# Optimization experiments

Measured on AMD Instinct MI355X. Metric: run time of the kernel, lower is better.

## Reference

```python
import jax, jax.numpy as jnp
import numpy as np

N_NODES = 100000
N_REL = 8
IN_DIM = 64
HID = 128
OUT = 64
N_EDGES = 640000


def setup_inputs() -> dict:
    key = jax.random.key(0)
    ks = jax.random.split(key, 24)

    def w(k, shape, fan_in):
        return jax.random.normal(k, shape, jnp.float32) / np.sqrt(fan_in).astype(np.float32)

    inp = {}
    inp["emb"] = jax.random.normal(ks[0], (N_NODES, IN_DIM), jnp.float32)
    dims = [(IN_DIM, HID), (HID, HID), (HID, HID // 2), (HID // 2, OUT)]
    for i, (di, do) in enumerate(dims, 1):
        inp[f"W{i}"] = w(ks[3 * i], (N_REL, di, do), di)      # per-relation weight
        inp[f"R{i}"] = w(ks[3 * i + 1], (di, do), di)          # root weight
        inp[f"B{i}"] = jnp.zeros((do,), jnp.float32)           # bias
    inp["g1"] = jnp.ones((HID,), jnp.float32)
    inp["b1"] = jnp.zeros((HID,), jnp.float32)
    inp["g2"] = jnp.ones((HID,), jnp.float32)
    inp["b2"] = jnp.zeros((HID,), jnp.float32)
    inp["ei"] = jax.random.randint(ks[20], (2, N_EDGES), 0, N_NODES, jnp.int32)
    inp["et"] = jax.random.randint(ks[21], (N_EDGES,), 0, N_REL, jnp.int32)
    return inp


def rgcn(x, ei, et, W, Wr, b):
    # PyG RGCNConv (aggr='mean'): out_i = x_i @ Wroot + b + sum_r mean_{j in N_r(i)} x_j @ W_r
    # Aggregate-then-transform: mean x[src] per (dst, rel) bin, then per-relation GEMM.
    n, r, d = x.shape[0], W.shape[0], x.shape[1]
    src, dst = ei[0], ei[1]
    seg = dst * r + et                                   # combined (node, relation) segment id
    agg = jax.ops.segment_sum(x[src], seg, num_segments=n * r)          # [N*R, d]
    cnt = jax.ops.segment_sum(jnp.ones((src.shape[0],), x.dtype), seg, num_segments=n * r)
    agg = (agg / jnp.maximum(cnt, 1.0)[:, None]).reshape(n, r, d)       # mean per relation
    return jnp.einsum('nri,rio->no', agg, W) + x @ Wr + b


def layer_norm(x, g, b, eps=1e-5):
    mu = jnp.mean(x, axis=-1, keepdims=True)
    var = jnp.mean((x - mu) ** 2, axis=-1, keepdims=True)
    return (x - mu) * jax.lax.rsqrt(var + eps) * g + b


def reference(emb, W1, R1, B1, W2, R2, B2, W3, R3, B3, W4, R4, B4, g1, b1, g2, b2, ei, et):
    # dropout is eval-mode identity
    x = jax.nn.relu(rgcn(emb, ei, et, W1, R1, B1))
    x = layer_norm(x, g1, b1)
    identity = x
    x = jax.nn.relu(rgcn(x, ei, et, W2, R2, B2))
    x = layer_norm(x + identity, g2, b2)
    x = jax.nn.relu(rgcn(x, ei, et, W3, R3, B3))
    return rgcn(x, ei, et, W4, R4, B4)
```

## Files before the change

kernel.cpp:

```cpp
#include <hip/hip_runtime.h>
#include <math.h>

#define NN 100000
#define NR 8
#define NE 640000
#define SEGN (NN * NR)
#define SPB 2048
#define NSB ((SEGN + SPB - 1) / SPB)

#define TILES 1563
#define HT1 782
#define HT2 781
#define HP1 (HT1 * 64)
#define HP2 (HT2 * 64)
#define HPF (TILES * 64)

typedef __attribute__((ext_vector_type(8))) __bf16 bf16x8;
typedef __attribute__((ext_vector_type(4))) float  f32x4;

__device__ __forceinline__ float bf2f(unsigned short b) {
    return __uint_as_float((unsigned)b << 16);
}
__device__ __forceinline__ unsigned short f2bf(float v) {
    __bf16 b = (__bf16)v;
    return __builtin_bit_cast(unsigned short, b);
}


__global__ __launch_bounds__(256) void count_kernel(
    const int* __restrict__ dst, const int* __restrict__ et, unsigned* __restrict__ cnt) {
    int e = blockIdx.x * 256 + threadIdx.x;
    if (e < NE) atomicAdd(&cnt[(size_t)et[e] * NN + dst[e]], 1u);
}

__global__ __launch_bounds__(256) void scan1_kernel(
    const unsigned* __restrict__ cnt, unsigned* __restrict__ bsum) {
    __shared__ unsigned red[256];
    int b = blockIdx.x, t = threadIdx.x;
    int i0 = b * SPB;
    unsigned s = 0;
#pragma unroll
    for (int k = 0; k < SPB / 256; ++k) {
        int i = i0 + k * 256 + t;
        if (i < SEGN) s += cnt[i];
    }
    red[t] = s;
    __syncthreads();
    for (int off = 128; off >= 1; off >>= 1) {
        if (t < off) red[t] += red[t + off];
        __syncthreads();
    }
    if (t == 0) bsum[b] = red[0];
}

__global__ __launch_bounds__(512) void scan2_kernel(
    unsigned* __restrict__ bsum, int* __restrict__ segoff) {
    __shared__ unsigned buf[512];
    int t = threadIdx.x;
    unsigned v = (t < NSB) ? bsum[t] : 0u;
    buf[t] = v;
    __syncthreads();
    for (int off = 1; off < 512; off <<= 1) {
        unsigned w = (t >= off) ? buf[t - off] : 0u;
        __syncthreads();
        buf[t] += w;
        __syncthreads();
    }
    if (t < NSB) bsum[t] = buf[t] - v;
    if (t == 0) segoff[SEGN] = NE;
}

__global__ __launch_bounds__(256) void scan3_kernel(
    const unsigned* __restrict__ cnt, const unsigned* __restrict__ bsum,
    int* __restrict__ segoff) {
    __shared__ unsigned lc[SPB];
    __shared__ unsigned tsum[256];
    int b = blockIdx.x, t = threadIdx.x;
    int i0 = b * SPB;
#pragma unroll
    for (int k = 0; k < SPB / 256; ++k) {
        int i = i0 + k * 256 + t;
        lc[k * 256 + t] = (i < SEGN) ? cnt[i] : 0u;
    }
    __syncthreads();
    unsigned s = 0;
#pragma unroll
    for (int k = 0; k < 8; ++k) s += lc[t * 8 + k];
    tsum[t] = s;
    __syncthreads();
    for (int off = 1; off < 256; off <<= 1) {
        unsigned w = (t >= off) ? tsum[t - off] : 0u;
        __syncthreads();
        tsum[t] += w;
        __syncthreads();
    }
    unsigned base = bsum[b] + tsum[t] - s;
#pragma unroll
    for (int k = 0; k < 8; ++k) {
        unsigned c = lc[t * 8 + k];
        lc[t * 8 + k] = base;
        base += c;
    }
    __syncthreads();
#pragma unroll
    for (int k = 0; k < SPB / 256; ++k) {
        int i = i0 + k * 256 + t;
        if (i < SEGN) segoff[i] = (int)lc[k * 256 + t];
    }
}

__global__ __launch_bounds__(256) void fill_kernel(
    const int* __restrict__ src, const int* __restrict__ dst, const int* __restrict__ et,
    const int* __restrict__ segoff, unsigned* __restrict__ cursor, int* __restrict__ esrc) {
    int e = blockIdx.x * 256 + threadIdx.x;
    if (e >= NE) return;
    int d = dst[e];
    int seg = et[e] * NN + d;
    int pos = segoff[seg] + (int)atomicAdd(&cursor[seg], 1u);
    esrc[pos] = src[e] | ((d & 3) << 17);
}


template <int D, int O>
__global__ __launch_bounds__(256) void pack_kernel(
    const float* __restrict__ W, const float* __restrict__ Wr, __bf16* __restrict__ Wp) {
    constexpr int KT = D / 32, NTN = O / 16;
    int idx = blockIdx.x * 256 + threadIdx.x;
    if (idx >= (NR + 1) * KT * NTN * 64) return;
    int l = idx & 63;
    int rest = idx >> 6;
    int nt = rest % NTN; rest /= NTN;
    int kt = rest % KT;
    int r  = rest / KT;
    const float* srcw = (r < NR) ? (W + (size_t)r * D * O) : Wr;
    int n  = nt * 16 + (l & 15);
    int k0 = kt * 32 + (l >> 4) * 8;
    bf16x8 v;
#pragma unroll
    for (int j = 0; j < 8; ++j) {
        int p  = k0 + j;
        int kd = (D == 128) ? ((p >> 1) + ((p & 1) << 6)) : p;
        v[j] = (__bf16)srcw[(size_t)kd * O + n];
    }
    *(bf16x8*)(Wp + (size_t)idx * 8) = v;
}


template <int D, int XF>
__global__ __launch_bounds__(256) void gather_kernel(
    const void* __restrict__ xin, const int* __restrict__ segoff,
    const int* __restrict__ esrc, ushort* __restrict__ agg,
    int nbase, int agg_off, int HP)
{
    int wv = threadIdx.x >> 6, ln = threadIdx.x & 63;
    int r  = blockIdx.y;
    int i0 = blockIdx.x * 16 + wv * 4;
    int n0 = nbase + i0;

    const float*    xf = (const float*)xin;
    const ushort*   xb = (const ushort*)xin;
    const unsigned* xs = (const unsigned*)xin;

    float ax[4] = {0, 0, 0, 0}, ay[4] = {0, 0, 0, 0};
    int eo[5];
#pragma unroll
    for (int k = 0; k <= 4; ++k) {
        int node = n0 + k; if (node > NN) node = NN;
        eo[k] = segoff[r * NN + node];
    }
    for (int ei = eo[0]; ei < eo[4]; ei += 4) {
        int nb = eo[4] - ei; if (nb > 4) nb = 4;
        int mm[4]; float vx[4], vy[4];
#pragma unroll
        for (int b = 0; b < 4; ++b) mm[b] = (b < nb) ? esrc[ei + b] : 0;
#pragma unroll
        for (int b = 0; b < 4; ++b) {
            if (b < nb) {
                int s = mm[b] & 0x1FFFF;
                if constexpr (XF == 0) {
                    vx[b] = xf[(size_t)s * 64 + ln];
                } else if constexpr (XF == 1) {
                    unsigned w = xs[(size_t)s * 64 + ln];
                    vx[b] = bf2f((unsigned short)(w & 0xFFFFu));
                    vy[b] = bf2f((unsigned short)(w >> 16));
                } else {
                    vx[b] = bf2f(xb[(size_t)s * 64 + ln]);
                }
            }
        }
#pragma unroll
        for (int b = 0; b < 4; ++b) {
            if (b < nb) {
                int k = mm[b] >> 17;
#pragma unroll
                for (int kk = 0; kk < 4; ++kk) {
                    ax[kk] += (kk == k) ? vx[b] : 0.0f;
                    if constexpr (D == 128) ay[kk] += (kk == k) ? vy[b] : 0.0f;
                }
            }
        }
    }
#pragma unroll
    for (int k = 0; k < 4; ++k) {
        int c = eo[k + 1] - eo[k];
        float sc = (c > 0) ? 1.0f / (float)c : 0.0f;
        size_t row = ((size_t)r * HP + agg_off + i0 + k) * D;
        if constexpr (D == 128) {
            unsigned st = (unsigned)f2bf(ax[k] * sc) | ((unsigned)f2bf(ay[k] * sc) << 16);
            *((unsigned*)(agg + row) + ln) = st;
        } else {
            agg[row + ln] = f2bf(ax[k] * sc);
        }
    }
}


template <int D, int O, int MODE, int XF, int OF>
__global__ __launch_bounds__(256) void gemm_layer(
    const ushort* __restrict__ agg, const __bf16* __restrict__ Wp,
    const float* __restrict__ bias, const float* __restrict__ gamma,
    const float* __restrict__ beta, const unsigned* __restrict__ xres,
    const void* __restrict__ xroot, void* __restrict__ outv, int base, int HP)
{
    constexpr int KT = D / 32, NTN = O / 16;
    int t = threadIdx.x, wv = t >> 6, ln = t & 63, lg = ln >> 4, lm = ln & 15;
    int i0 = blockIdx.x * 64;

    f32x4 acc[NTN];
#pragma unroll
    for (int nt = 0; nt < NTN; ++nt)
#pragma unroll
        for (int q = 0; q < 4; ++q) acc[nt][q] = 0.0f;

    const ushort* abase = agg + ((size_t)(i0 + wv * 16 + lm)) * D + lg * 8;

#pragma unroll 1
    for (int r = 0; r < 8; ++r) {
        const ushort* ar = abase + (size_t)r * HP * D;
        const __bf16* bp = Wp + (((size_t)(r * KT) * NTN) << 9) + (ln << 3);
#pragma unroll
        for (int kt = 0; kt < KT; ++kt) {
            bf16x8 A = *(const bf16x8*)(ar + kt * 32);
            const __bf16* bpk = bp + (((size_t)(kt * NTN)) << 9);
#pragma unroll
            for (int nt = 0; nt < NTN; ++nt) {
                bf16x8 B = *(const bf16x8*)(bpk + ((size_t)nt << 9));
                acc[nt] = __builtin_amdgcn_mfma_f32_16x16x32_bf16(A, B, acc[nt], 0, 0, 0);
            }
        }
    }
    {
        int nrow = base + i0 + wv * 16 + lm;
        if (nrow >= NN) nrow = NN - 1;
        const __bf16* bp = Wp + (((size_t)(8 * KT) * NTN) << 9) + (ln << 3);
#pragma unroll
        for (int kt = 0; kt < KT; ++kt) {
            bf16x8 A;
            if constexpr (XF == 0) {
                const float* xp = (const float*)xroot + (size_t)nrow * 64 + kt * 32 + lg * 8;
                f32x4 a0 = *(const f32x4*)xp;
                f32x4 a1 = *(const f32x4*)(xp + 4);
#pragma unroll
                for (int j = 0; j < 4; ++j) { A[j] = (__bf16)a0[j]; A[j + 4] = (__bf16)a1[j]; }
            } else if constexpr (XF == 1) {
                A = *(const bf16x8*)((const ushort*)xroot + (size_t)nrow * 128 + kt * 32 + lg * 8);
            } else {
                A = *(const bf16x8*)((const ushort*)xroot + (size_t)nrow * 64 + kt * 32 + lg * 8);
            }
            const __bf16* bpk = bp + (((size_t)(kt * NTN)) << 9);
#pragma unroll
            for (int nt = 0; nt < NTN; ++nt) {
                bf16x8 B = *(const bf16x8*)(bpk + ((size_t)nt << 9));
                acc[nt] = __builtin_amdgcn_mfma_f32_16x16x32_bf16(A, B, acc[nt], 0, 0, 0);
            }
        }
    }

    float bb[NTN], gg[NTN], be[NTN];
#pragma unroll
    for (int nt = 0; nt < NTN; ++nt) {
        bb[nt] = bias[nt * 16 + lm];
        if constexpr (MODE <= 1) {
            gg[nt] = gamma[nt * 16 + lm];
            be[nt] = beta[nt * 16 + lm];
        } else {
            gg[nt] = 0.0f; be[nt] = 0.0f;
        }
    }
#pragma unroll
    for (int q = 0; q < 4; ++q) {
        int row = wv * 16 + lg * 4 + q;
        int n = base + i0 + row;
        int nc = (n < NN) ? n : 0;
        float v[NTN];
#pragma unroll
        for (int nt = 0; nt < NTN; ++nt) {
            v[nt] = acc[nt][q] + bb[nt];
            if constexpr (MODE <= 2) v[nt] = fmaxf(v[nt], 0.0f);
            if constexpr (MODE == 1) {
                unsigned w = xres[(size_t)nc * 64 + (nt & 3) * 16 + lm];
                v[nt] += bf2f((unsigned short)((nt < 4) ? (w & 0xFFFFu) : (w >> 16)));
            }
        }
        if constexpr (MODE <= 1) {
            float s1 = 0.0f, s2 = 0.0f;
#pragma unroll
            for (int nt = 0; nt < NTN; ++nt) { s1 += v[nt]; s2 += v[nt] * v[nt]; }
#pragma unroll
            for (int off = 1; off < 16; off <<= 1) {
                s1 += __shfl_xor(s1, off, 64);
                s2 += __shfl_xor(s2, off, 64);
            }
            float mu  = s1 * (1.0f / O);
            float var = s2 * (1.0f / O) - mu * mu;
            float rs  = rsqrtf(var + 1e-5f);
#pragma unroll
            for (int nt = 0; nt < NTN; ++nt) v[nt] = (v[nt] - mu) * rs * gg[nt] + be[nt];
        }
        if (n < NN) {
            if constexpr (OF == 0) {
#pragma unroll
                for (int nt = 0; nt < NTN; ++nt)
                    __builtin_nontemporal_store(
                        v[nt], (float*)outv + (size_t)n * O + nt * 16 + lm);
            } else if constexpr (OF == 1) {
#pragma unroll
                for (int nt = 0; nt < 4; ++nt)
                    ((unsigned*)outv)[(size_t)n * 64 + nt * 16 + lm] =
                        (unsigned)f2bf(v[nt]) | ((unsigned)f2bf(v[nt + 4]) << 16);
            } else {
#pragma unroll
                for (int nt = 0; nt < NTN; ++nt)
                    ((ushort*)outv)[(size_t)n * 64 + nt * 16 + lm] = f2bf(v[nt]);
            }
        }
    }
}


extern "C" void kernel_launch(void* const* d_in, const int* in_sizes, int n_in,
                              void* d_out, int out_size, void* d_ws, size_t ws_size,
                              hipStream_t stream) {
    const float* emb = (const float*)d_in[0];
    const float* W1  = (const float*)d_in[1];
    const float* R1  = (const float*)d_in[2];
    const float* B1  = (const float*)d_in[3];
    const float* W2  = (const float*)d_in[4];
    const float* R2  = (const float*)d_in[5];
    const float* B2  = (const float*)d_in[6];
    const float* W3  = (const float*)d_in[7];
    const float* R3  = (const float*)d_in[8];
    const float* B3  = (const float*)d_in[9];
    const float* W4  = (const float*)d_in[10];
    const float* R4  = (const float*)d_in[11];
    const float* B4  = (const float*)d_in[12];
    const float* g1  = (const float*)d_in[13];
    const float* b1  = (const float*)d_in[14];
    const float* g2  = (const float*)d_in[15];
    const float* b2  = (const float*)d_in[16];
    const int*   ei  = (const int*)d_in[17];
    const int*   et  = (const int*)d_in[18];
    const int* srcp = ei;
    const int* dstp = ei + NE;

    char* ws = (char*)d_ws;
    if (ws_size < 185734160u) return;
    int*      segoff = (int*)(ws + 0);
    int*      esrc   = (int*)(ws + 3200016);
    __bf16*   Wp1    = (__bf16*)(ws + 5760016);
    __bf16*   Wp2    = (__bf16*)(ws + 5907472);
    __bf16*   Wp3    = (__bf16*)(ws + 6202384);
    __bf16*   Wp4    = (__bf16*)(ws + 6349840);
    void*     x1     = (void*)(ws + 6423568);
    void*     x2     = (void*)(ws + 32023568);
    void*     x3     = (void*)(ws + 57623568);
    ushort*   agg    = (ushort*)(ws + 70423568);
    unsigned* cnt    = (unsigned*)(ws + 70423568);
    unsigned* cursor = (unsigned*)(ws + 73623568);
    unsigned* bsum   = (unsigned*)(ws + 76823568);
    float*    outp   = (float*)d_out;

    hipMemsetAsync(cnt, 0, 3200000, stream);
    hipMemsetAsync(cursor, 0, 3200000, stream);

    count_kernel<<<(NE + 255) / 256, 256, 0, stream>>>(dstp, et, cnt);
    scan1_kernel<<<NSB, 256, 0, stream>>>(cnt, bsum);
    scan2_kernel<<<1, 512, 0, stream>>>(bsum, segoff);
    scan3_kernel<<<NSB, 256, 0, stream>>>(cnt, bsum, segoff);
    fill_kernel<<<(NE + 255) / 256, 256, 0, stream>>>(
        srcp, dstp, et, segoff, cursor, esrc);

    pack_kernel<64, 128><<<(9 * 2 * 8 * 64 + 255) / 256, 256, 0, stream>>>(W1, R1, Wp1);
    pack_kernel<128, 128><<<(9 * 4 * 8 * 64 + 255) / 256, 256, 0, stream>>>(W2, R2, Wp2);
    pack_kernel<128, 64><<<(9 * 4 * 4 * 64 + 255) / 256, 256, 0, stream>>>(W3, R3, Wp3);
    pack_kernel<64, 64><<<(9 * 2 * 4 * 64 + 255) / 256, 256, 0, stream>>>(W4, R4, Wp4);

    gather_kernel<64, 0><<<dim3(HP1 / 16, 8), 256, 0, stream>>>(emb, segoff, esrc, agg, 0, 0, HPF);
    gather_kernel<64, 0><<<dim3(HP2 / 16, 8), 256, 0, stream>>>(emb, segoff, esrc, agg, HP1, HP1, HPF);
    gemm_layer<64, 128, 0, 0, 1><<<TILES, 256, 0, stream>>>(
        agg, Wp1, B1, g1, b1, nullptr, emb, x1, 0, HPF);

    gather_kernel<128, 1><<<dim3(25024 / 16, 8), 256, 0, stream>>>(x1, segoff, esrc, agg, 0, 0, HP1);
    gather_kernel<128, 1><<<dim3(25024 / 16, 8), 256, 0, stream>>>(x1, segoff, esrc, agg, 25024, 25024, HP1);
    gemm_layer<128, 128, 1, 1, 1><<<HT1, 256, 0, stream>>>(
        agg, Wp2, B2, g2, b2, (const unsigned*)x1, x1, x2, 0, HP1);
    gather_kernel<128, 1><<<dim3(25024 / 16, 8), 256, 0, stream>>>(x1, segoff, esrc, agg, HP1, 0, HP2);
    gather_kernel<128, 1><<<dim3(24960 / 16, 8), 256, 0, stream>>>(x1, segoff, esrc, agg, HP1 + 25024, 25024, HP2);
    gemm_layer<128, 128, 1, 1, 1><<<HT2, 256, 0, stream>>>(
        agg, Wp2, B2, g2, b2, (const unsigned*)x1, x1, x2, HP1, HP2);

    gather_kernel<128, 1><<<dim3(25024 / 16, 8), 256, 0, stream>>>(x2, segoff, esrc, agg, 0, 0, HP1);
    gather_kernel<128, 1><<<dim3(25024 / 16, 8), 256, 0, stream>>>(x2, segoff, esrc, agg, 25024, 25024, HP1);
    gemm_layer<128, 64, 2, 1, 2><<<HT1, 256, 0, stream>>>(
        agg, Wp3, B3, nullptr, nullptr, nullptr, x2, x3, 0, HP1);
    gather_kernel<128, 1><<<dim3(25024 / 16, 8), 256, 0, stream>>>(x2, segoff, esrc, agg, HP1, 0, HP2);
    gather_kernel<128, 1><<<dim3(24960 / 16, 8), 256, 0, stream>>>(x2, segoff, esrc, agg, HP1 + 25024, 25024, HP2);
    gemm_layer<128, 64, 2, 1, 2><<<HT2, 256, 0, stream>>>(
        agg, Wp3, B3, nullptr, nullptr, nullptr, x2, x3, HP1, HP2);

    gather_kernel<64, 2><<<dim3(HP1 / 16, 8), 256, 0, stream>>>(x3, segoff, esrc, agg, 0, 0, HPF);
    gather_kernel<64, 2><<<dim3(HP2 / 16, 8), 256, 0, stream>>>(x3, segoff, esrc, agg, HP1, HP1, HPF);
    gemm_layer<64, 64, 3, 2, 0><<<TILES, 256, 0, stream>>>(
        agg, Wp4, B4, nullptr, nullptr, nullptr, x3, outp, 0, HPF);
}
```

Baseline: 782.5 us.

## Use one-wave GEMM blocks and prefetch next relation's aggregated rows

The GEMM kernel now runs one 64-lane wave per block handling 16 rows instead of four waves handling 64 rows, giving four times as many blocks. Root-feature A operands are loaded up front, and the aggregated A fragments for the next relation are double-buffered in registers so their loads overlap the current relation's MFMAs. This targets load latency and scheduling granularity in the memory-bound GEMM stage, at the cost of more registers per wave and no sharing of weight loads across waves within a block.

```diff
diff --git a/kernel.cpp b/kernel.cpp
--- a/kernel.cpp
+++ b/kernel.cpp
@@ -216,15 +216,15 @@
 
 
 template <int D, int O, int MODE, int XF, int OF>
-__global__ __launch_bounds__(256) void gemm_layer(
+__global__ __launch_bounds__(64) void gemm_layer(
     const ushort* __restrict__ agg, const __bf16* __restrict__ Wp,
     const float* __restrict__ bias, const float* __restrict__ gamma,
     const float* __restrict__ beta, const unsigned* __restrict__ xres,
     const void* __restrict__ xroot, void* __restrict__ outv, int base, int HP)
 {
     constexpr int KT = D / 32, NTN = O / 16;
-    int t = threadIdx.x, wv = t >> 6, ln = t & 63, lg = ln >> 4, lm = ln & 15;
-    int i0 = blockIdx.x * 64;
+    int ln = threadIdx.x, lg = ln >> 4, lm = ln & 15;
+    int i0 = blockIdx.x * 16;
 
     f32x4 acc[NTN];
 #pragma unroll
@@ -232,46 +232,67 @@
 #pragma unroll
         for (int q = 0; q < 4; ++q) acc[nt][q] = 0.0f;
 
-    const ushort* abase = agg + ((size_t)(i0 + wv * 16 + lm)) * D + lg * 8;
-
-#pragma unroll 1
-    for (int r = 0; r < 8; ++r) {
-        const ushort* ar = abase + (size_t)r * HP * D;
-        const __bf16* bp = Wp + (((size_t)(r * KT) * NTN) << 9) + (ln << 3);
+    bf16x8 Aroot[KT];
+    {
+        int nrow = base + i0 + lm;
+        if (nrow >= NN) nrow = NN - 1;
 #pragma unroll
         for (int kt = 0; kt < KT; ++kt) {
-            bf16x8 A = *(const bf16x8*)(ar + kt * 32);
-            const __bf16* bpk = bp + (((size_t)(kt * NTN)) << 9);
-#pragma unroll
-            for (int nt = 0; nt < NTN; ++nt) {
-                bf16x8 B = *(const bf16x8*)(bpk + ((size_t)nt << 9));
-                acc[nt] = __builtin_amdgcn_mfma_f32_16x16x32_bf16(A, B, acc[nt], 0, 0, 0);
-            }
-        }
-    }
-    {
-        int nrow = base + i0 + wv * 16 + lm;
-        if (nrow >= NN) nrow = NN - 1;
-        const __bf16* bp = Wp + (((size_t)(8 * KT) * NTN) << 9) + (ln << 3);
-#pragma unroll
-        for (int kt = 0; kt < KT; ++kt) {
-            bf16x8 A;
             if constexpr (XF == 0) {
                 const float* xp = (const float*)xroot + (size_t)nrow * 64 + kt * 32 + lg * 8;
                 f32x4 a0 = *(const f32x4*)xp;
                 f32x4 a1 = *(const f32x4*)(xp + 4);
 #pragma unroll
-                for (int j = 0; j < 4; ++j) { A[j] = (__bf16)a0[j]; A[j + 4] = (__bf16)a1[j]; }
+                for (int j = 0; j < 4; ++j) {
+                    Aroot[kt][j] = (__bf16)a0[j];
+                    Aroot[kt][j + 4] = (__bf16)a1[j];
+                }
             } else if constexpr (XF == 1) {
-                A = *(const bf16x8*)((const ushort*)xroot + (size_t)nrow * 128 + kt * 32 + lg * 8);
+                Aroot[kt] = *(const bf16x8*)((const ushort*)xroot +
+                                             (size_t)nrow * 128 + kt * 32 + lg * 8);
             } else {
-                A = *(const bf16x8*)((const ushort*)xroot + (size_t)nrow * 64 + kt * 32 + lg * 8);
-            }
+                Aroot[kt] = *(const bf16x8*)((const ushort*)xroot +
+                                             (size_t)nrow * 64 + kt * 32 + lg * 8);
+            }
+        }
+    }
+
+    const ushort* abase = agg + ((size_t)(i0 + lm)) * D + lg * 8;
+    bf16x8 Acur[KT], Anxt[KT];
+#pragma unroll
+    for (int kt = 0; kt < KT; ++kt)
+        Acur[kt] = *(const bf16x8*)(abase + kt * 32);
+
+#pragma unroll 1
+    for (int r = 0; r < 8; ++r) {
+        if (r < 7) {
+            const ushort* an = abase + (size_t)(r + 1) * HP * D;
+#pragma unroll
+            for (int kt = 0; kt < KT; ++kt)
+                Anxt[kt] = *(const bf16x8*)(an + kt * 32);
+        }
+        const __bf16* bp = Wp + (((size_t)(r * KT) * NTN) << 9) + (ln << 3);
+#pragma unroll
+        for (int kt = 0; kt < KT; ++kt) {
             const __bf16* bpk = bp + (((size_t)(kt * NTN)) << 9);
 #pragma unroll
             for (int nt = 0; nt < NTN; ++nt) {
                 bf16x8 B = *(const bf16x8*)(bpk + ((size_t)nt << 9));
-                acc[nt] = __builtin_amdgcn_mfma_f32_16x16x32_bf16(A, B, acc[nt], 0, 0, 0);
+                acc[nt] = __builtin_amdgcn_mfma_f32_16x16x32_bf16(Acur[kt], B, acc[nt], 0, 0, 0);
+            }
+        }
+#pragma unroll
+        for (int kt = 0; kt < KT; ++kt) Acur[kt] = Anxt[kt];
+    }
+    {
+        const __bf16* bp = Wp + (((size_t)(8 * KT) * NTN) << 9) + (ln << 3);
+#pragma unroll
+        for (int kt = 0; kt < KT; ++kt) {
+            const __bf16* bpk = bp + (((size_t)(kt * NTN)) << 9);
+#pragma unroll
+            for (int nt = 0; nt < NTN; ++nt) {
+                bf16x8 B = *(const bf16x8*)(bpk + ((size_t)nt << 9));
+                acc[nt] = __builtin_amdgcn_mfma_f32_16x16x32_bf16(Aroot[kt], B, acc[nt], 0, 0, 0);
             }
         }
     }
@@ -289,7 +310,7 @@
     }
 #pragma unroll
     for (int q = 0; q < 4; ++q) {
-        int row = wv * 16 + lg * 4 + q;
+        int row = lg * 4 + q;
         int n = base + i0 + row;
         int nc = (n < NN) ? n : 0;
         float v[NTN];
@@ -397,29 +418,29 @@
 
     gather_kernel<64, 0><<<dim3(HP1 / 16, 8), 256, 0, stream>>>(emb, segoff, esrc, agg, 0, 0, HPF);
     gather_kernel<64, 0><<<dim3(HP2 / 16, 8), 256, 0, stream>>>(emb, segoff, esrc, agg, HP1, HP1, HPF);
-    gemm_layer<64, 128, 0, 0, 1><<<TILES, 256, 0, stream>>>(
+    gemm_layer<64, 128, 0, 0, 1><<<HPF / 16, 64, 0, stream>>>(
         agg, Wp1, B1, g1, b1, nullptr, emb, x1, 0, HPF);
 
     gather_kernel<128, 1><<<dim3(25024 / 16, 8), 256, 0, stream>>>(x1, segoff, esrc, agg, 0, 0, HP1);
     gather_kernel<128, 1><<<dim3(25024 / 16, 8), 256, 0, stream>>>(x1, segoff, esrc, agg, 25024, 25024, HP1);
-    gemm_layer<128, 128, 1, 1, 1><<<HT1, 256, 0, stream>>>(
+    gemm_layer<128, 128, 1, 1, 1><<<HP1 / 16, 64, 0, stream>>>(
         agg, Wp2, B2, g2, b2, (const unsigned*)x1, x1, x2, 0, HP1);
     gather_kernel<128, 1><<<dim3(25024 / 16, 8), 256, 0, stream>>>(x1, segoff, esrc, agg, HP1, 0, HP2);
     gather_kernel<128, 1><<<dim3(24960 / 16, 8), 256, 0, stream>>>(x1, segoff, esrc, agg, HP1 + 25024, 25024, HP2);
-    gemm_layer<128, 128, 1, 1, 1><<<HT2, 256, 0, stream>>>(
+    gemm_layer<128, 128, 1, 1, 1><<<HP2 / 16, 64, 0, stream>>>(
         agg, Wp2, B2, g2, b2, (const unsigned*)x1, x1, x2, HP1, HP2);
 
     gather_kernel<128, 1><<<dim3(25024 / 16, 8), 256, 0, stream>>>(x2, segoff, esrc, agg, 0, 0, HP1);
     gather_kernel<128, 1><<<dim3(25024 / 16, 8), 256, 0, stream>>>(x2, segoff, esrc, agg, 25024, 25024, HP1);
-    gemm_layer<128, 64, 2, 1, 2><<<HT1, 256, 0, stream>>>(
+    gemm_layer<128, 64, 2, 1, 2><<<HP1 / 16, 64, 0, stream>>>(
         agg, Wp3, B3, nullptr, nullptr, nullptr, x2, x3, 0, HP1);
     gather_kernel<128, 1><<<dim3(25024 / 16, 8), 256, 0, stream>>>(x2, segoff, esrc, agg, HP1, 0, HP2);
     gather_kernel<128, 1><<<dim3(24960 / 16, 8), 256, 0, stream>>>(x2, segoff, esrc, agg, HP1 + 25024, 25024, HP2);
-    gemm_layer<128, 64, 2, 1, 2><<<HT2, 256, 0, stream>>>(
+    gemm_layer<128, 64, 2, 1, 2><<<HP2 / 16, 64, 0, stream>>>(
         agg, Wp3, B3, nullptr, nullptr, nullptr, x2, x3, HP1, HP2);
 
     gather_kernel<64, 2><<<dim3(HP1 / 16, 8), 256, 0, stream>>>(x3, segoff, esrc, agg, 0, 0, HPF);
     gather_kernel<64, 2><<<dim3(HP2 / 16, 8), 256, 0, stream>>>(x3, segoff, esrc, agg, HP1, HP1, HPF);
-    gemm_layer<64, 64, 3, 2, 0><<<TILES, 256, 0, stream>>>(
+    gemm_layer<64, 64, 3, 2, 0><<<HPF / 16, 64, 0, stream>>>(
         agg, Wp4, B4, nullptr, nullptr, nullptr, x3, outp, 0, HPF);
 }
```

New measurement: 701.5 us. 10.4% less time.
